# Optimization experiments

Measured on AMD Instinct MI355X. Metric: run time of the kernel, lower is better.

Reference implementation:

```python
import jax, jax.numpy as jnp
import numpy as np

EPS = float(np.finfo(np.float32).eps)
H = 256          # hidden_size
K = 10           # num_event_types
B, S = 32, 4096  # batch, seq_len


def _linear_params(kw, kb, fan_in, fan_out):
    # torch nn.Linear default init (uniform +-1/sqrt(fan_in)), then abs + clamp(min=eps)
    bound = 1.0 / np.sqrt(fan_in)
    w = jnp.clip(jnp.abs(jax.random.uniform(kw, (fan_out, fan_in), minval=-bound, maxval=bound, dtype=jnp.float32)), EPS)
    b = jnp.clip(jnp.abs(jax.random.uniform(kb, (fan_out,), minval=-bound, maxval=bound, dtype=jnp.float32)), EPS)
    return w, b


def setup_inputs() -> dict:
    key = jax.random.key(0)
    ks = jax.random.split(key, 12)
    w1, b1 = _linear_params(ks[0], ks[1], 1, H)        # layer_dense_1
    w2, b2 = _linear_params(ks[2], ks[3], 2 * H, H)    # layer_dense_2
    wA, bA = _linear_params(ks[4], ks[5], H, H)        # module_list[0]
    wB, bB = _linear_params(ks[6], ks[7], H, H)        # module_list[1]
    w3, b3 = _linear_params(ks[8], ks[9], H, K)        # layer_dense_3 linear
    hidden_states = jax.random.normal(ks[10], (B, S, H), dtype=jnp.float32)
    time_delta_seqs = jax.random.uniform(ks[11], (B, S), dtype=jnp.float32)
    return dict(hidden_states=hidden_states, time_delta_seqs=time_delta_seqs,
                w1=w1, b1=b1, w2=w2, b2=b2, wA=wA, bA=bA, wB=wB, bB=bB, w3=w3, b3=b3)


def _cumul_hazard(td, h, w1, b1, w2, b2, wA, bA, wB, bB, w3, b3):
    # layer_dense_1: Linear(1 -> H) on td[..., None]
    t = td[..., None] * w1[:, 0] + b1                      # [B,S,H]
    out = jnp.tanh(jnp.concatenate([h, t], axis=-1) @ w2.T + b2)  # [B,S,H]
    out = jnp.tanh(out @ wA.T + bA)
    out = jnp.tanh(out @ wB.T + bB)
    return jax.nn.softplus(out @ w3.T + b3)                # [B,S,K]


def reference(hidden_states, time_delta_seqs, w1, b1, w2, b2, wA, bA, wB, bB, w3, b3):
    f = lambda td: _cumul_hazard(td, hidden_states, w1, b1, w2, b2, wA, bA, wB, bB, w3, b3)
    # Each output element depends only on its own t[b,s] (elementwise in time),
    # so a single forward-mode JVP with tangent=ones yields the exact per-element
    # derivative for ALL event types at once (fuses torch's per-type grad loop).
    integral_lambda, d_dt = jax.jvp(f, (time_delta_seqs,), (jnp.ones_like(time_delta_seqs),))
    # torch takes grad of .mean() over [B,S], which scales the derivative by 1/(B*S)
    derivative_integral_lambda = d_dt / time_delta_seqs.size
    return integral_lambda, derivative_integral_lambda
```

## Files before the change

kernel.cpp:

```cpp
#include <hip/hip_runtime.h>
#include <hip/hip_bf16.h>
#include <stdint.h>

typedef __bf16 bf16x8 __attribute__((ext_vector_type(8)));
typedef float  f32x4  __attribute__((ext_vector_type(4)));

#define MFMA16(a,b,c) __builtin_amdgcn_mfma_f32_16x16x32_bf16((a),(b),(c),0,0,0)

static constexpr int H_   = 256;
static constexpr int KEV  = 10;
static constexpr int NTOK = 32 * 4096;
static constexpr int NCHUNK = 48;

__device__ __forceinline__ float fast_tanh(float x){
    x = fminf(fmaxf(x, -9.0f), 9.0f);
    float e = __builtin_amdgcn_exp2f(2.8853900817779268f * x);
    return (e - 1.0f) * __builtin_amdgcn_rcpf(e + 1.0f);
}

__device__ __forceinline__ void cp16(void* lds, const void* g){
    auto l = reinterpret_cast<__attribute__((address_space(3))) uint32_t*>(
                 (uint32_t)reinterpret_cast<uintptr_t>(lds));
    auto s = reinterpret_cast<const __attribute__((address_space(1))) uint32_t*>(
                 reinterpret_cast<uintptr_t>(g));
    __builtin_amdgcn_global_load_lds(s, l, 16, 0, 0);
}

__device__ __forceinline__ bf16x8 cvtFrag(const float* p){
    f32x4 a = *(const f32x4*)p;
    f32x4 b = *(const f32x4*)(p + 4);
    bf16x8 r;
    #pragma unroll
    for (int j = 0; j < 4; ++j){ r[j] = (__bf16)a[j]; r[4 + j] = (__bf16)b[j]; }
    return r;
}

__global__ void prep_vc(const float* __restrict__ w1, const float* __restrict__ b1,
                        const float* __restrict__ w2, const float* __restrict__ b2,
                        float* __restrict__ vc){
    int j = blockIdx.x * 4 + (threadIdx.x >> 6);
    int l = threadIdx.x & 63;
    const float* row = w2 + (size_t)j * (2 * H_) + H_;
    float v = 0.f, cc = 0.f;
    #pragma unroll
    for (int i = 0; i < 4; ++i){
        int k = l + 64 * i;
        float w = row[k];
        v  += w * w1[k];
        cc += w * b1[k];
    }
    #pragma unroll
    for (int off = 32; off; off >>= 1){
        v  += __shfl_down(v,  off, 64);
        cc += __shfl_down(cc, off, 64);
    }
    if (l == 0){ vc[j] = v; vc[H_ + j] = cc + b2[j]; }
}

__global__ void prep_pack(const float* __restrict__ w2, const float* __restrict__ wA,
                          const float* __restrict__ wB, __hip_bfloat16* __restrict__ pk){
    int b  = blockIdx.x;
    int L  = b >> 4, n0 = b & 15;
    const float* W = (L == 0) ? w2 : ((L == 1) ? wA : wB);
    int K = (L == 0) ? 2 * H_ : H_;
    __hip_bfloat16* dst = pk + (size_t)b * 4096;
    int t = threadIdx.x;
    #pragma unroll
    for (int u = 0; u < 2; ++u){
        int slot = t * 2 + u;
        int s = slot >> 6, q = (slot >> 4) & 3, c = slot & 15;
        const float* src = W + (size_t)(n0 * 16 + c) * K + 32 * s + 8 * q;
        #pragma unroll
        for (int j = 0; j < 8; ++j) dst[slot * 8 + j] = __float2bfloat16(src[j]);
    }
}

__global__ __launch_bounds__(256, 2) void chfn_kernel(
    const float* __restrict__ hs, const float* __restrict__ td,
    const __hip_bfloat16* __restrict__ wpk,
    const float* __restrict__ bA, const float* __restrict__ bB,
    const float* __restrict__ w3, const float* __restrict__ b3,
    const float* __restrict__ vc,
    float* __restrict__ out)
{
    __shared__ __hip_bfloat16 sA[4 * 16 * H_];
    __shared__ __hip_bfloat16 sD[4 * 16 * H_];
    __shared__ __hip_bfloat16 wls[2][4096];

    const int tid  = threadIdx.x;
    const int wave = tid >> 6;
    const int lane = tid & 63;
    const int q    = lane >> 4;
    const int c    = lane & 15;
    const int tokenBase = blockIdx.x * 64 + wave * 16;
    const int wrow = wave * 16;

    const float* hrow = hs + (size_t)(tokenBase + c) * H_ + 8 * q;
    f32x4 h0[8], h1[8];
    #pragma unroll
    for (int s = 0; s < 8; ++s){
        h0[s] = *(const f32x4*)(hrow + 32 * s);
        h1[s] = *(const f32x4*)(hrow + 32 * s + 4);
    }

    #pragma unroll
    for (int j = 0; j < 2; ++j){
        int i = wave * 2 + j;
        cp16((char*)&wls[0][0] + i * 1024, (const char*)wpk + i * 1024 + lane * 16);
    }

    float myTd = td[tokenBase + c];
    float tdv[4];
    #pragma unroll
    for (int r = 0; r < 4; ++r) tdv[r] = __shfl(myTd, q * 4 + r, 64);

    bf16x8 aF[8], aB[8];
    #pragma unroll
    for (int s = 0; s < 8; ++s){
        bf16x8 rr;
        #pragma unroll
        for (int j = 0; j < 4; ++j){ rr[j] = (__bf16)h0[s][j]; rr[4 + j] = (__bf16)h1[s][j]; }
        aF[s] = rr;
    }

    __syncthreads();

    int g = 0;
    #pragma unroll 1
    for (int n0 = 0; n0 < 16; ++n0, ++g){
        const __hip_bfloat16* cur = wls[g & 1];
        {
            const char* src = (const char*)(wpk + (size_t)(g + 1) * 4096);
            #pragma unroll
            for (int j = 0; j < 2; ++j){
                int i = wave * 2 + j;
                cp16((char*)&wls[(g + 1) & 1][0] + i * 1024, src + i * 1024 + lane * 16);
            }
        }
        f32x4 f0 = {0.f,0.f,0.f,0.f};
        #pragma unroll
        for (int s = 0; s < 8; ++s){
            bf16x8 bv = *(const bf16x8*)(cur + ((s * 4 + q) * 16 + c) * 8);
            f0 = MFMA16(aF[s], bv, f0);
        }
        int n = n0 * 16 + c;
        float v1n = vc[n], c1n = vc[H_ + n];
        #pragma unroll
        for (int r = 0; r < 4; ++r){
            float x  = f0[r] + tdv[r] * v1n + c1n;
            float th = fast_tanh(x);
            float dd = (1.0f - th * th) * v1n;
            int row = 4 * q + r;
            int off = (wrow + row) * H_ + ((((n >> 3) + row) & 31) << 3) + (n & 7);
            sA[off] = __float2bfloat16(th);
            sD[off] = __float2bfloat16(dd);
        }
        __syncthreads();
    }

    const float* bias2[2] = {bA, bB};
    #pragma unroll 1
    for (int L = 0; L < 2; ++L){
        const float* bias = bias2[L];
        const __hip_bfloat16* arow = sA + (wrow + c) * H_;
        const __hip_bfloat16* drow = sD + (wrow + c) * H_;
        #pragma unroll
        for (int s = 0; s < 8; ++s){
            int ch = (((4 * s + q) + c) & 31) << 3;
            aF[s] = *(const bf16x8*)(arow + ch);
            aB[s] = *(const bf16x8*)(drow + ch);
        }
        #pragma unroll 1
        for (int n0 = 0; n0 < 16; ++n0, ++g){
            const __hip_bfloat16* cur = wls[g & 1];
            if (g + 1 < NCHUNK){
                const char* src = (const char*)(wpk + (size_t)(g + 1) * 4096);
                #pragma unroll
                for (int j = 0; j < 2; ++j){
                    int i = wave * 2 + j;
                    cp16((char*)&wls[(g + 1) & 1][0] + i * 1024, src + i * 1024 + lane * 16);
                }
            }
            f32x4 f0 = {0.f,0.f,0.f,0.f}, g0 = {0.f,0.f,0.f,0.f};
            #pragma unroll
            for (int s = 0; s < 8; ++s){
                bf16x8 bv = *(const bf16x8*)(cur + ((s * 4 + q) * 16 + c) * 8);
                f0 = MFMA16(aF[s], bv, f0);
                g0 = MFMA16(aB[s], bv, g0);
            }
            int n = n0 * 16 + c;
            float bn = bias[n];
            #pragma unroll
            for (int r = 0; r < 4; ++r){
                float th = fast_tanh(f0[r] + bn);
                float dd = (1.0f - th * th) * g0[r];
                int row = 4 * q + r;
                int off = (wrow + row) * H_ + ((((n >> 3) + row) & 31) << 3) + (n & 7);
                sA[off] = __float2bfloat16(th);
                sD[off] = __float2bfloat16(dd);
            }
            __syncthreads();
        }
    }

    {
        const __hip_bfloat16* arow = sA + (wrow + c) * H_;
        const __hip_bfloat16* drow = sD + (wrow + c) * H_;
        #pragma unroll
        for (int s = 0; s < 8; ++s){
            int ch = (((4 * s + q) + c) & 31) << 3;
            aF[s] = *(const bf16x8*)(arow + ch);
            aB[s] = *(const bf16x8*)(drow + ch);
        }
        int crow = (c < KEV) ? c : 0;
        const float* wp0 = w3 + (size_t)crow * H_ + 8 * q;
        f32x4 f0 = {0.f,0.f,0.f,0.f}, g0 = {0.f,0.f,0.f,0.f};
        #pragma unroll
        for (int s = 0; s < 8; ++s){
            bf16x8 bv = cvtFrag(wp0 + 32 * s);
            f0 = MFMA16(aF[s], bv, f0);
            g0 = MFMA16(aB[s], bv, g0);
        }
        if (c < KEV){
            float bn = b3[c];
            #pragma unroll
            for (int r = 0; r < 4; ++r){
                float z  = f0[r] + bn;
                float a  = fabsf(z);
                float e  = __builtin_amdgcn_exp2f(-1.4426950408889634f * a);
                float sp = fmaxf(z, 0.f) +
                           0.69314718055994531f * __builtin_amdgcn_logf(1.0f + e);
                float sg = __builtin_amdgcn_rcpf(1.0f + e);
                sg = (z >= 0.f) ? sg : 1.0f - sg;
                float dv = sg * g0[r] * (1.0f / 131072.0f);
                size_t token = tokenBase + 4 * q + r;
                out[token * KEV + c] = sp;
                out[(size_t)NTOK * KEV + token * KEV + c] = dv;
            }
        }
    }
}

extern "C" void kernel_launch(void* const* d_in, const int* in_sizes, int n_in,
                              void* d_out, int out_size, void* d_ws, size_t ws_size,
                              hipStream_t stream){
    const float* hs = (const float*)d_in[0];
    const float* td = (const float*)d_in[1];
    const float* w1 = (const float*)d_in[2];
    const float* b1 = (const float*)d_in[3];
    const float* w2 = (const float*)d_in[4];
    const float* b2 = (const float*)d_in[5];
    const float* wA = (const float*)d_in[6];
    const float* bA = (const float*)d_in[7];
    const float* wB = (const float*)d_in[8];
    const float* bB = (const float*)d_in[9];
    const float* w3 = (const float*)d_in[10];
    const float* b3 = (const float*)d_in[11];

    float*          vc  = (float*)d_ws;
    __hip_bfloat16* wpk = (__hip_bfloat16*)((char*)d_ws + 4096);
    float*          outp = (float*)d_out;

    prep_vc  <<<64, 256, 0, stream>>>(w1, b1, w2, b2, vc);
    prep_pack<<<48, 256, 0, stream>>>(w2, wA, wB, wpk);
    chfn_kernel<<<NTOK / 64, 256, 0, stream>>>(hs, td, wpk, bA, bB, w3, b3, vc, outp);
}
```

Before: 339.8 us.

## Transpose MFMA operands, split accumulators, use Padé tanh and vectorized stores

Swaps the A/B operands of every MFMA so each lane holds four consecutive output features for one token. This allows vectorized bf16x4 LDS writes of activations and vectorized float2 output stores instead of scalar scattered writes. Each GEMM is split into two independent accumulator chains to shorten MFMA dependency latency. The exp-based tanh is replaced by a clamped rational Padé approximation. The td shuffles are dropped, and biases and vc are loaded as float4. The Padé tanh is less accurate at large arguments, and the extra accumulators add register pressure.

```diff
diff --git a/kernel.cpp b/kernel.cpp
--- a/kernel.cpp
+++ b/kernel.cpp
@@ -3,7 +3,9 @@
 #include <stdint.h>
 
 typedef __bf16 bf16x8 __attribute__((ext_vector_type(8)));
+typedef __bf16 bf16x4 __attribute__((ext_vector_type(4)));
 typedef float  f32x4  __attribute__((ext_vector_type(4)));
+typedef float  f32x2  __attribute__((ext_vector_type(2)));
 
 #define MFMA16(a,b,c) __builtin_amdgcn_mfma_f32_16x16x32_bf16((a),(b),(c),0,0,0)
 
@@ -12,10 +14,12 @@
 static constexpr int NTOK = 32 * 4096;
 static constexpr int NCHUNK = 48;
 
-__device__ __forceinline__ float fast_tanh(float x){
-    x = fminf(fmaxf(x, -9.0f), 9.0f);
-    float e = __builtin_amdgcn_exp2f(2.8853900817779268f * x);
-    return (e - 1.0f) * __builtin_amdgcn_rcpf(e + 1.0f);
+__device__ __forceinline__ float ptanh(float x){
+    float t = x * x;
+    float n = fmaf(t, t + 105.0f, 945.0f);
+    float d = fmaf(t, fmaf(t, 15.0f, 420.0f), 945.0f);
+    float r = x * n * __builtin_amdgcn_rcpf(d);
+    return fminf(1.0f, fmaxf(-1.0f, r));
 }
 
 __device__ __forceinline__ void cp16(void* lds, const void* g){
@@ -110,9 +114,6 @@
     }
 
     float myTd = td[tokenBase + c];
-    float tdv[4];
-    #pragma unroll
-    for (int r = 0; r < 4; ++r) tdv[r] = __shfl(myTd, q * 4 + r, 64);
 
     bf16x8 aF[8], aB[8];
     #pragma unroll
@@ -137,24 +138,29 @@
                 cp16((char*)&wls[(g + 1) & 1][0] + i * 1024, src + i * 1024 + lane * 16);
             }
         }
-        f32x4 f0 = {0.f,0.f,0.f,0.f};
-        #pragma unroll
-        for (int s = 0; s < 8; ++s){
-            bf16x8 bv = *(const bf16x8*)(cur + ((s * 4 + q) * 16 + c) * 8);
-            f0 = MFMA16(aF[s], bv, f0);
-        }
-        int n = n0 * 16 + c;
-        float v1n = vc[n], c1n = vc[H_ + n];
+        f32x4 fa = {0.f,0.f,0.f,0.f}, fb = {0.f,0.f,0.f,0.f};
+        #pragma unroll
+        for (int s = 0; s < 4; ++s){
+            bf16x8 bv0 = *(const bf16x8*)(cur + ((s * 4 + q) * 16 + c) * 8);
+            bf16x8 bv1 = *(const bf16x8*)(cur + (((s + 4) * 4 + q) * 16 + c) * 8);
+            fa = MFMA16(bv0, aF[s],     fa);
+            fb = MFMA16(bv1, aF[s + 4], fb);
+        }
+        int nb = n0 * 16 + 4 * q;
+        f32x4 v4 = *(const f32x4*)(vc + nb);
+        f32x4 c4 = *(const f32x4*)(vc + H_ + nb);
+        bf16x4 pa, pd;
         #pragma unroll
         for (int r = 0; r < 4; ++r){
-            float x  = f0[r] + tdv[r] * v1n + c1n;
-            float th = fast_tanh(x);
-            float dd = (1.0f - th * th) * v1n;
-            int row = 4 * q + r;
-            int off = (wrow + row) * H_ + ((((n >> 3) + row) & 31) << 3) + (n & 7);
-            sA[off] = __float2bfloat16(th);
-            sD[off] = __float2bfloat16(dd);
-        }
+            float x  = (fa[r] + fb[r]) + fmaf(myTd, v4[r], c4[r]);
+            float th = ptanh(x);
+            float dd = fmaf(-th, th, 1.0f) * v4[r];
+            pa[r] = (__bf16)th; pd[r] = (__bf16)dd;
+        }
+        int ch  = 2 * n0 + (q >> 1);
+        int off = (wrow + c) * H_ + (((ch + c) & 31) << 3) + ((q & 1) << 2);
+        *(bf16x4*)((void*)(sA + off)) = pa;
+        *(bf16x4*)((void*)(sD + off)) = pd;
         __syncthreads();
     }
 
@@ -166,9 +172,9 @@
         const __hip_bfloat16* drow = sD + (wrow + c) * H_;
         #pragma unroll
         for (int s = 0; s < 8; ++s){
-            int ch = (((4 * s + q) + c) & 31) << 3;
-            aF[s] = *(const bf16x8*)(arow + ch);
-            aB[s] = *(const bf16x8*)(drow + ch);
+            int chn = (((4 * s + q) + c) & 31) << 3;
+            aF[s] = *(const bf16x8*)(arow + chn);
+            aB[s] = *(const bf16x8*)(drow + chn);
         }
         #pragma unroll 1
         for (int n0 = 0; n0 < 16; ++n0, ++g){
@@ -181,24 +187,30 @@
                     cp16((char*)&wls[(g + 1) & 1][0] + i * 1024, src + i * 1024 + lane * 16);
                 }
             }
-            f32x4 f0 = {0.f,0.f,0.f,0.f}, g0 = {0.f,0.f,0.f,0.f};
+            f32x4 fa = {0.f,0.f,0.f,0.f}, fb = {0.f,0.f,0.f,0.f};
+            f32x4 ga = {0.f,0.f,0.f,0.f}, gb = {0.f,0.f,0.f,0.f};
             #pragma unroll
-            for (int s = 0; s < 8; ++s){
-                bf16x8 bv = *(const bf16x8*)(cur + ((s * 4 + q) * 16 + c) * 8);
-                f0 = MFMA16(aF[s], bv, f0);
-                g0 = MFMA16(aB[s], bv, g0);
-            }
-            int n = n0 * 16 + c;
-            float bn = bias[n];
+            for (int s = 0; s < 4; ++s){
+                bf16x8 bv0 = *(const bf16x8*)(cur + ((s * 4 + q) * 16 + c) * 8);
+                bf16x8 bv1 = *(const bf16x8*)(cur + (((s + 4) * 4 + q) * 16 + c) * 8);
+                fa = MFMA16(bv0, aF[s],     fa);
+                ga = MFMA16(bv0, aB[s],     ga);
+                fb = MFMA16(bv1, aF[s + 4], fb);
+                gb = MFMA16(bv1, aB[s + 4], gb);
+            }
+            int nb = n0 * 16 + 4 * q;
+            f32x4 b4 = *(const f32x4*)(bias + nb);
+            bf16x4 pa, pd;
             #pragma unroll
             for (int r = 0; r < 4; ++r){
-                float th = fast_tanh(f0[r] + bn);
-                float dd = (1.0f - th * th) * g0[r];
-                int row = 4 * q + r;
-                int off = (wrow + row) * H_ + ((((n >> 3) + row) & 31) << 3) + (n & 7);
-                sA[off] = __float2bfloat16(th);
-                sD[off] = __float2bfloat16(dd);
-            }
+                float th = ptanh((fa[r] + fb[r]) + b4[r]);
+                float dd = fmaf(-th, th, 1.0f) * (ga[r] + gb[r]);
+                pa[r] = (__bf16)th; pd[r] = (__bf16)dd;
+            }
+            int ch  = 2 * n0 + (q >> 1);
+            int off = (wrow + c) * H_ + (((ch + c) & 31) << 3) + ((q & 1) << 2);
+            *(bf16x4*)((void*)(sA + off)) = pa;
+            *(bf16x4*)((void*)(sD + off)) = pd;
             __syncthreads();
         }
     }
@@ -208,35 +220,48 @@
         const __hip_bfloat16* drow = sD + (wrow + c) * H_;
         #pragma unroll
         for (int s = 0; s < 8; ++s){
-            int ch = (((4 * s + q) + c) & 31) << 3;
-            aF[s] = *(const bf16x8*)(arow + ch);
-            aB[s] = *(const bf16x8*)(drow + ch);
+            int chn = (((4 * s + q) + c) & 31) << 3;
+            aF[s] = *(const bf16x8*)(arow + chn);
+            aB[s] = *(const bf16x8*)(drow + chn);
         }
         int crow = (c < KEV) ? c : 0;
         const float* wp0 = w3 + (size_t)crow * H_ + 8 * q;
-        f32x4 f0 = {0.f,0.f,0.f,0.f}, g0 = {0.f,0.f,0.f,0.f};
-        #pragma unroll
-        for (int s = 0; s < 8; ++s){
-            bf16x8 bv = cvtFrag(wp0 + 32 * s);
-            f0 = MFMA16(aF[s], bv, f0);
-            g0 = MFMA16(aB[s], bv, g0);
-        }
-        if (c < KEV){
-            float bn = b3[c];
-            #pragma unroll
-            for (int r = 0; r < 4; ++r){
-                float z  = f0[r] + bn;
-                float a  = fabsf(z);
-                float e  = __builtin_amdgcn_exp2f(-1.4426950408889634f * a);
-                float sp = fmaxf(z, 0.f) +
-                           0.69314718055994531f * __builtin_amdgcn_logf(1.0f + e);
-                float sg = __builtin_amdgcn_rcpf(1.0f + e);
-                sg = (z >= 0.f) ? sg : 1.0f - sg;
-                float dv = sg * g0[r] * (1.0f / 131072.0f);
-                size_t token = tokenBase + 4 * q + r;
-                out[token * KEV + c] = sp;
-                out[(size_t)NTOK * KEV + token * KEV + c] = dv;
-            }
+        f32x4 fa = {0.f,0.f,0.f,0.f}, fb = {0.f,0.f,0.f,0.f};
+        f32x4 ga = {0.f,0.f,0.f,0.f}, gb = {0.f,0.f,0.f,0.f};
+        #pragma unroll
+        for (int s = 0; s < 4; ++s){
+            bf16x8 bv0 = cvtFrag(wp0 + 32 * s);
+            bf16x8 bv1 = cvtFrag(wp0 + 32 * (s + 4));
+            fa = MFMA16(bv0, aF[s],     fa);
+            ga = MFMA16(bv0, aB[s],     ga);
+            fb = MFMA16(bv1, aF[s + 4], fb);
+            gb = MFMA16(bv1, aB[s + 4], gb);
+        }
+        int fbase = 4 * q;
+        size_t token = tokenBase + c;
+        float sp[4], dv[4];
+        #pragma unroll
+        for (int r = 0; r < 4; ++r){
+            int fi  = fbase + r;
+            float bn = b3[(fi < KEV) ? fi : (KEV - 1)];
+            float z  = (fa[r] + fb[r]) + bn;
+            float a  = fabsf(z);
+            float e  = __builtin_amdgcn_exp2f(-1.4426950408889634f * a);
+            sp[r] = fmaxf(z, 0.f) + 0.69314718055994531f * __builtin_amdgcn_logf(1.0f + e);
+            float sg = __builtin_amdgcn_rcpf(1.0f + e);
+            sg = (z >= 0.f) ? sg : 1.0f - sg;
+            dv[r] = sg * (ga[r] + gb[r]) * (1.0f / 131072.0f);
+        }
+        float* o0 = out + token * KEV + fbase;
+        float* o1 = out + (size_t)NTOK * KEV + token * KEV + fbase;
+        if (q < 2){
+            *(f32x2*)o0       = (f32x2){sp[0], sp[1]};
+            *(f32x2*)(o0 + 2) = (f32x2){sp[2], sp[3]};
+            *(f32x2*)o1       = (f32x2){dv[0], dv[1]};
+            *(f32x2*)(o1 + 2) = (f32x2){dv[2], dv[3]};
+        } else if (q == 2){
+            *(f32x2*)o0 = (f32x2){sp[0], sp[1]};
+            *(f32x2*)o1 = (f32x2){dv[0], dv[1]};
         }
     }
 }
```

New measurement: 345.6 us. No clear change (+1.7%).
